# Kernel optimization log

Hardware: AMD Instinct MI355X
Metric: run time of the kernel (lower is better)

Reference implementation:

```python
import jax, jax.numpy as jnp
import numpy as np

EPS = 1e-6


def _rmsnorm(x, w, eps=EPS):
    # x: (..., d); normalize over last dim
    ms = jnp.mean(jnp.square(x), axis=-1, keepdims=True)
    return x * jax.lax.rsqrt(ms + eps) * w


def setup_inputs() -> dict:
    key = jax.random.key(0)
    ks = jax.random.split(key, 5)
    B, S, D = 2, 2048, 2048
    n_heads, n_kv = 16, 4
    d_head = D // n_heads  # 128
    sd = 1.0 / np.sqrt(D)
    return {
        "x": jax.random.normal(ks[0], (B, S, D), dtype=jnp.float32),
        "wq": jax.random.normal(ks[1], (D, n_heads * d_head), dtype=jnp.float32) * sd,
        "wk": jax.random.normal(ks[2], (D, n_kv * d_head), dtype=jnp.float32) * sd,
        "wv": jax.random.normal(ks[3], (D, n_kv * d_head), dtype=jnp.float32) * sd,
        "wo": jax.random.normal(ks[4], (D, D), dtype=jnp.float32) * sd,
        "q_norm_w": jnp.ones((d_head,), dtype=jnp.float32),
        "k_norm_w": jnp.ones((d_head,), dtype=jnp.float32),
    }


def reference(x, wq, wk, wv, wo, q_norm_w, k_norm_w):
    B, S, D = x.shape
    n_heads, n_kv = 16, 4
    groups = n_heads // n_kv
    d_head = D // n_heads

    # QKV projections (bias=False)
    q = (x @ wq).reshape(B, S, n_kv, groups, d_head)  # q heads grouped by kv head
    k = (x @ wk).reshape(B, S, n_kv, d_head)
    v = (x @ wv).reshape(B, S, n_kv, d_head)

    # qk RMSNorm over d_head
    q = _rmsnorm(q, q_norm_w)
    k = _rmsnorm(k, k_norm_w)

    # GQA attention without materializing expanded K/V:
    # scores: (B, n_kv, groups, S_q, S_k)
    scale = 1.0 / jnp.sqrt(jnp.asarray(d_head, dtype=x.dtype))
    scores = jnp.einsum('bskgd,btkd->bkgst', q, k) * scale
    causal = jnp.tril(jnp.ones((S, S), dtype=bool))
    scores = jnp.where(causal, scores, jnp.asarray(-jnp.inf, dtype=scores.dtype))
    attn = jax.nn.softmax(scores, axis=-1)
    out = jnp.einsum('bkgst,btkd->bskgd', attn, v)  # (B, S, n_kv, groups, d_head)
    out = out.reshape(B, S, D)
    return out @ wo
```

## Files before the change

kernel.cpp:

```cpp
#include <hip/hip_runtime.h>
#include <hip/hip_bf16.h>
#include <stdint.h>

typedef unsigned short u16;
typedef __attribute__((ext_vector_type(8))) short short8;
typedef __attribute__((ext_vector_type(4))) float f32x4;
typedef __attribute__((ext_vector_type(16))) float f32x16;

__device__ __forceinline__ u16 f2bf(float f){
  union { __hip_bfloat16 h; u16 u; } v; v.h = __float2bfloat16(f); return v.u;
}
__device__ __forceinline__ float bf2f(u16 h){
  union { uint32_t u; float f; } v; v.u = ((uint32_t)h) << 16;
  return v.f;
}
__device__ __forceinline__ f32x4 mfma16(short8 a, short8 b, f32x4 c){
  return __builtin_amdgcn_mfma_f32_16x16x32_bf16(a, b, c, 0, 0, 0);
}
__device__ __forceinline__ f32x16 mfma32(short8 a, short8 b, f32x16 c){
  return __builtin_amdgcn_mfma_f32_32x32x16_bf16(a, b, c, 0, 0, 0);
}
__device__ __forceinline__ void gl_lds16(const u16* g, u16* l){
  __builtin_amdgcn_global_load_lds((const __attribute__((address_space(1))) void*)g,
                                   (__attribute__((address_space(3))) void*)l, 16, 0, 0);
}
template<int N> __device__ __forceinline__ void waitvm(){
  if constexpr (N==0) asm volatile("s_waitcnt vmcnt(0)" ::: "memory");
  else if constexpr (N==2) asm volatile("s_waitcnt vmcnt(2)" ::: "memory");
  else if constexpr (N==4) asm volatile("s_waitcnt vmcnt(4)" ::: "memory");
  else if constexpr (N==8) asm volatile("s_waitcnt vmcnt(8)" ::: "memory");
  else static_assert(N==0 || N==2 || N==4 || N==8, "unsupported vmcnt");
}
__device__ __forceinline__ void phase_sep(){
  __builtin_amdgcn_sched_barrier(0);
  __builtin_amdgcn_s_barrier();
  __builtin_amdgcn_sched_barrier(0);
}
__device__ __forceinline__ uint32_t cvtpk(float lo, float hi){
  uint32_t r;
  asm("v_cvt_pk_bf16_f32 %0, %1, %2" : "=v"(r) : "v"(lo), "v"(hi));
  return r;
}

__global__ __launch_bounds__(256) void prep(const float* __restrict__ x,
    const float* __restrict__ wq, const float* __restrict__ wk,
    const float* __restrict__ wv, const float* __restrict__ wo,
    u16* __restrict__ xbf, u16* __restrict__ wqkvT, u16* __restrict__ woT)
{
  __shared__ float tile[32][33];
  int bid = blockIdx.x;
  const int tid = threadIdx.x;
  if (bid < 8192){
    const int i = bid*256 + tid;
    const float4 v = ((const float4*)x)[i];
    ushort4 pk;
    pk.x = f2bf(v.x); pk.y = f2bf(v.y); pk.z = f2bf(v.z); pk.w = f2bf(v.w);
    ((ushort4*)xbf)[i] = pk;
    return;
  }
  bid -= 8192;
  const float* src; u16* dst; int C, bx, by;
  if (bid < 4096){ src = wq; dst = wqkvT; C = 2048; bx = bid & 63; by = bid >> 6; }
  else if (bid < 8192){ bid -= 4096; src = wo; dst = woT; C = 2048; bx = bid & 63; by = bid >> 6; }
  else if (bid < 9216){ bid -= 8192; src = wk; dst = wqkvT + 2048*2048; C = 512; bx = bid & 15; by = bid >> 4; }
  else { bid -= 9216; src = wv; dst = wqkvT + 2560*2048; C = 512; bx = bid & 15; by = bid >> 4; }
  const int R = 2048;
  const int tx = tid & 31, ty = tid >> 5;
  const int c0 = bx << 5, r0 = by << 5;
  #pragma unroll
  for (int i=0;i<4;i++)
    tile[ty + (i<<3)][tx] = src[(size_t)(r0 + ty + (i<<3))*C + c0 + tx];
  __syncthreads();
  #pragma unroll
  for (int i=0;i<4;i++)
    dst[(size_t)(c0 + ty + (i<<3))*R + r0 + tx] = f2bf(tile[tx][ty + (i<<3)]);
}

__global__ __launch_bounds__(256) void v_transpose(const u16* __restrict__ qkv,
    u16* __restrict__ vT)
{
  __shared__ u16 tile[32][33];
  const int tx = threadIdx.x, ty = threadIdx.y;
  const int s0 = blockIdx.x << 5, d0 = blockIdx.y << 5;
  const int bk = blockIdx.z; const int b = bk >> 2, kv = bk & 3;
  const u16* src = qkv + (size_t)b*2048*3072 + 2560 + kv*128;
  #pragma unroll
  for (int i=0;i<4;i++)
    tile[ty + (i<<3)][tx] = src[(size_t)(s0 + ty + (i<<3))*3072 + d0 + tx];
  __syncthreads();
  u16* dst = vT + (size_t)((b<<2)+kv)*128*2048;
  #pragma unroll
  for (int i=0;i<4;i++)
    dst[(size_t)(d0 + ty + (i<<3))*2048 + s0 + tx] = tile[tx][ty + (i<<3)];
}

__global__ __launch_bounds__(256) void rmsnorm_k(u16* __restrict__ qkv,
    const float* __restrict__ kw)
{
  const int lane = threadIdx.x & 63;
  const int rid = blockIdx.x*4 + (threadIdx.x >> 6);
  const int row = rid >> 2;
  const int slot = rid & 3;
  u16* p = qkv + (size_t)row*3072 + 2048 + slot*128 + (lane<<1);
  const u16 r0 = p[0], r1 = p[1];
  const float a = bf2f(r0), c = bf2f(r1);
  float ss = a*a + c*c;
  #pragma unroll
  for (int off=1; off<64; off<<=1) ss += __shfl_xor(ss, off);
  const float sc = rsqrtf(ss*(1.0f/128.0f) + 1e-6f);
  const float w0 = kw[lane<<1], w1 = kw[(lane<<1)+1];
  p[0] = f2bf(a*sc*w0);
  p[1] = f2bf(c*sc*w1);
}

template<int BM, int CBF16>
__global__ __launch_bounds__(512, 2) void gemm8(const u16* __restrict__ A,
    const u16* __restrict__ BT, void* __restrict__ Cp,
    int M, int N, int K, int ldc)
{
  constexpr int MF   = BM/32;
  constexpr int MQ   = MF/2;
  constexpr int AH   = BM/2;
  constexpr int ASZ  = AH*64;
  constexpr int DBUF = 2*ASZ + 16384;
  constexpr int WV   = (BM==256) ? 4 : 2;
  __shared__ u16 lds[2*DBUF];
  const int tid = threadIdx.x;
  const int w = tid >> 6, lane = tid & 63;
  const int l15 = lane & 15, lg = lane >> 4;
  const int wm = w >> 2, wn = w & 3;
  const int nbx = N >> 8;
  const int nwg = gridDim.x;
  int bid = blockIdx.x;
  bid = (bid & 7) * (nwg >> 3) + (bid >> 3);
  const int m0 = (bid / nbx) * BM;
  const int n0 = (bid % nbx) << 8;

  const u16* gA0 = A  + (size_t)m0*K;
  const u16* gA1 = gA0 + (size_t)AH*K;
  const u16* gB0 = BT + (size_t)n0*K;
  const u16* gB1 = gB0 + (size_t)128*K;

  auto slotA = [&](int d, int h)->u16*{ return lds + d*DBUF + h*ASZ; };
  auto slotB = [&](int d, int h)->u16*{ return lds + d*DBUF + 2*ASZ + h*8192; };

  auto stage_half = [&](const u16* gbase, int kt, u16* sbase, int rows){
    const int iters = rows >> 6;
    for (int i=0;i<iters;i++){
      const int p = (i<<9) + tid;
      const int row = p>>3, sg = (p&7) ^ (row&7);
      gl_lds16(gbase + (size_t)row*K + (kt<<6) + (sg<<3), sbase + (p<<3));
    }
  };
  auto stA = [&](int kt, int d){ stage_half(gA0, kt, slotA(d,0), AH);
                                 stage_half(gA1, kt, slotA(d,1), AH); };
  auto stB = [&](int kt, int d){ stage_half(gB0, kt, slotB(d,0), 128);
                                 stage_half(gB1, kt, slotB(d,1), 128); };
  auto frag_at = [&](const u16* buf, int lrow, int kk)->short8{
    const int s = ((kk<<2)+lg) ^ (lrow&7);
    return *(const short8*)(buf + (((lrow<<3)+s)<<3));
  };

  short8 af[MQ][2], bfe[2][2], bfo[2][2];
  f32x4 acc[MF][4];
  #pragma unroll
  for (int m=0;m<MF;m++)
    #pragma unroll
    for (int n=0;n<4;n++) acc[m][n] = (f32x4){0.f,0.f,0.f,0.f};

  const int bh = wn>>1;
  const int brow0 = ((wn&1)<<6) + l15;

  auto rd_a = [&](const u16* buf, int mq){
    #pragma unroll
    for (int m=0;m<MQ;m++)
      #pragma unroll
      for (int kk=0;kk<2;kk++)
        af[m][kk] = frag_at(buf, mq*(BM>>2) + (m<<4) + l15, kk);
  };
  auto rd_b = [&](const u16* buf, int nq, short8 (*dst)[2]){
    #pragma unroll
    for (int n=0;n<2;n++)
      #pragma unroll
      for (int kk=0;kk<2;kk++)
        dst[n][kk] = frag_at(buf, brow0 + (nq<<5) + (n<<4), kk);
  };
  auto do_mfma = [&](int mb, int nb, short8 (*bf)[2]){
    __builtin_amdgcn_s_setprio(1);
    #pragma unroll
    for (int m=0;m<MQ;m++)
      #pragma unroll
      for (int n=0;n<2;n++)
        #pragma unroll
        for (int kk=0;kk<2;kk++)
          acc[mb+m][nb+n] = mfma16(af[m][kk], bf[n][kk], acc[mb+m][nb+n]);
    __builtin_amdgcn_s_setprio(0);
  };

  stA(0,0); stB(0,0); stA(1,1);
  waitvm<WV>();
  phase_sep();

  const int niter = K >> 7;
  for (int i=0; i<niter; ++i){
    const bool full = (i+1 < niter);
    const int t1 = 2*i+1;
    rd_a(slotA(0,wm), 0); rd_b(slotB(0,bh), 0, bfe);
    stB(t1, 1);
    phase_sep();
    do_mfma(0, 0, bfe);
    phase_sep();
    rd_b(slotB(0,bh), 1, bfo);
    phase_sep();
    do_mfma(0, 2, bfo);
    phase_sep();
    rd_a(slotA(0,wm), 1);
    phase_sep();
    do_mfma(MQ, 2, bfo);
    phase_sep();
    rd_b(slotB(0,bh), 0, bfe);
    if (full) stA(t1+1, 0);
    phase_sep();
    do_mfma(MQ, 0, bfe);
    if (full) waitvm<WV>(); else waitvm<0>();
    phase_sep();
    rd_a(slotA(1,wm), 0); rd_b(slotB(1,bh), 0, bfe);
    if (full) stB(t1+1, 0);
    phase_sep();
    do_mfma(0, 0, bfe);
    phase_sep();
    rd_b(slotB(1,bh), 1, bfo);
    phase_sep();
    do_mfma(0, 2, bfo);
    phase_sep();
    rd_a(slotA(1,wm), 1);
    phase_sep();
    do_mfma(MQ, 2, bfo);
    phase_sep();
    rd_b(slotB(1,bh), 0, bfe);
    if (full) stA(t1+2, 1);
    phase_sep();
    do_mfma(MQ, 0, bfe);
    if (full) waitvm<WV>();
    phase_sep();
  }

  #pragma unroll
  for (int m=0;m<MF;m++){
    #pragma unroll
    for (int n=0;n<4;n++){
      const int col = n0 + (wn<<6) + (n<<4) + l15;
      #pragma unroll
      for (int r=0;r<4;r++){
        const int row = m0 + wm*AH + (m<<4) + (lg<<2) + r;
        if (CBF16) ((u16*)Cp)[(size_t)row*ldc + col] = f2bf(acc[m][n][r]);
        else       ((float*)Cp)[(size_t)row*ldc + col] = acc[m][n][r];
      }
    }
  }
}

__global__ __launch_bounds__(256, 2) void attn_kernel(const u16* __restrict__ qkv,
    const u16* __restrict__ vT, const float* __restrict__ qw,
    u16* __restrict__ aout)
{
  __shared__ u16 Klds[2][8192];
  __shared__ u16 Vlds[8192];
  const int tid = threadIdx.x;
  const int w = tid >> 6, lane = tid & 63;
  const int l31 = lane & 31, hi = lane >> 5;
  const int bx = blockIdx.x, h = blockIdx.y, b = blockIdx.z;
  const int qI = b ? bx : (15 - bx);
  const int kvh = h >> 2;
  const int qb = qI*128 + (w<<5);
  const int nt = 2*qI + 2;

  const u16* qkvb = qkv + (size_t)b*2048*3072;
  short8 qf[8];
  {
    const u16* qp = qkvb + (size_t)(qb + l31)*3072 + h*128 + hi*8;
    #pragma unroll
    for (int kk=0;kk<8;kk++) qf[kk] = *(const short8*)(qp + kk*16);
    float ss = 0.f;
    #pragma unroll
    for (int kk=0;kk<8;kk++)
      #pragma unroll
      for (int e=0;e<8;e++){
        const float v = bf2f((u16)qf[kk][e]);
        ss += v*v;
      }
    ss += __shfl_xor(ss, 32);
    const float sc = rsqrtf(ss*(1.0f/128.0f) + 1e-6f) * 0.1275187952317199f;
    #pragma unroll
    for (int kk=0;kk<8;kk++){
      #pragma unroll
      for (int e=0;e<8;e++){
        const float wv_ = qw[kk*16 + hi*8 + e];
        qf[kk][e] = (short)f2bf(bf2f((u16)qf[kk][e]) * sc * wv_);
      }
    }
  }
  f32x16 oacc[4];
  #pragma unroll
  for (int d=0;d<4;d++)
    #pragma unroll
    for (int r=0;r<16;r++) oacc[d][r] = 0.f;
  float m_run = -__builtin_inff(), lsum = 0.f;

  const u16* kb_ = qkvb + 2048 + kvh*128;
  const u16* vb_ = vT + (size_t)((b<<2)+kvh)*128*2048;

  auto stageK = [&](int t, int buf){
    #pragma unroll
    for (int i=0;i<4;i++){
      const int u = (i<<8) + tid;
      const int row = u>>4, d0 = (u&15) ^ (row&15);
      gl_lds16(kb_ + (size_t)((t<<6)+row)*3072 + (d0<<3), &Klds[buf][u<<3]);
    }
  };
  auto stageV = [&](int t){
    #pragma unroll
    for (int i=0;i<4;i++){
      const int u = (i<<8) + tid;
      const int rp = u>>4, z = (u&15) ^ (rp&15);
      const int d = (rp<<1) + (z>>3), k8 = z&7;
      gl_lds16(vb_ + (size_t)d*2048 + (t<<6) + (k8<<3), &Vlds[u<<3]);
    }
  };

  stageK(0, 0);
  int kbuf = 0;
  for (int t=0; t<nt; ++t){
    const bool pre = (t+1 < nt);
    stageV(t);
    if (pre) stageK(t+1, kbuf^1);
    if (pre) waitvm<8>(); else waitvm<4>();
    phase_sep();
    const int t0 = t<<6;
    f32x16 s0, s1;
    #pragma unroll
    for (int r=0;r<16;r++){ s0[r] = 0.f; s1[r] = 0.f; }
    #pragma unroll
    for (int kk=0;kk<8;kk++){
      const int d0 = (kk<<1) + hi;
      const short8 k0 = *(const short8*)&Klds[kbuf][((l31<<4) + (d0 ^ (l31&15)))<<3];
      s0 = mfma32(k0, qf[kk], s0);
      const int r1 = 32 + l31;
      const short8 k1 = *(const short8*)&Klds[kbuf][((r1<<4) + (d0 ^ (r1&15)))<<3];
      s1 = mfma32(k1, qf[kk], s1);
    }
    if (t0 + 63 > qb){
      const int qrel = qb + l31 - t0;
      #pragma unroll
      for (int r=0;r<16;r++){
        const int kloc = (r&3) + ((r>>2)<<3) + (hi<<2);
        if (kloc      > qrel) s0[r] = -__builtin_inff();
        if (kloc + 32 > qrel) s1[r] = -__builtin_inff();
      }
    }
    float t8[8];
    #pragma unroll
    for (int i=0;i<8;i++) t8[i] = fmaxf(fmaxf(s0[i], s0[i+8]), fmaxf(s1[i], s1[i+8]));
    #pragma unroll
    for (int i=0;i<4;i++) t8[i] = fmaxf(t8[i], t8[i+4]);
    float mx = fmaxf(fmaxf(t8[0],t8[1]), fmaxf(t8[2],t8[3]));
    mx = fmaxf(mx, __shfl_xor(mx, 32));
    const bool noskip = !__all(mx - m_run <= 8.0f);
    const float mnew = noskip ? fmaxf(m_run, mx) : m_run;
    float rs = 0.f;
    #pragma unroll
    for (int i=0;i<16;i++){
      s0[i] = __builtin_amdgcn_exp2f(s0[i] - mnew);
      s1[i] = __builtin_amdgcn_exp2f(s1[i] - mnew);
      rs += s0[i] + s1[i];
    }
    rs += __shfl_xor(rs, 32);
    if (noskip){
      const float corr = __builtin_amdgcn_exp2f(m_run - mnew);
      m_run = mnew;
      lsum = lsum*corr + rs;
      #pragma unroll
      for (int r=0;r<16;r++){
        const float cr = __shfl(corr, (r&3) + ((r>>2)<<3) + (hi<<2));
        #pragma unroll
        for (int db=0;db<4;db++) oacc[db][r] *= cr;
      }
    } else {
      lsum += rs;
    }
    uint32_t paw[4][4];
    #pragma unroll
    for (int kk=0;kk<4;kk++){
      const int base = (kk&1)<<3;
      float v0,v1,v2,v3,v4,v5,v6,v7;
      if (kk<2){ v0=s0[base+0]; v1=s0[base+1]; v2=s0[base+2]; v3=s0[base+3];
                 v4=s0[base+4]; v5=s0[base+5]; v6=s0[base+6]; v7=s0[base+7]; }
      else     { v0=s1[base+0]; v1=s1[base+1]; v2=s1[base+2]; v3=s1[base+3];
                 v4=s1[base+4]; v5=s1[base+5]; v6=s1[base+6]; v7=s1[base+7]; }
      uint32_t a0 = cvtpk(v0, v1), a1 = cvtpk(v2, v3);
      uint32_t b0 = cvtpk(v4, v5), b1 = cvtpk(v6, v7);
      asm volatile("v_permlane32_swap_b32 %0, %1" : "+v"(a0), "+v"(b0));
      asm volatile("v_permlane32_swap_b32 %0, %1" : "+v"(a1), "+v"(b1));
      paw[kk][0] = a0; paw[kk][1] = a1; paw[kk][2] = b0; paw[kk][3] = b1;
    }
    if (pre) waitvm<4>(); else waitvm<0>();
    phase_sep();
    #pragma unroll
    for (int kk=0;kk<4;kk++){
      union { uint32_t w[4]; short8 v; } pu;
      pu.w[0]=paw[kk][0]; pu.w[1]=paw[kk][1]; pu.w[2]=paw[kk][2]; pu.w[3]=paw[kk][3];
      const short8 pa = pu.v;
      #pragma unroll
      for (int db=0;db<4;db++){
        const int d = (db<<5) + l31, rp = d>>1;
        const int sl = (((d&1)<<3) | ((kk<<1)+hi)) ^ (rp&15);
        const short8 vv = *(const short8*)&Vlds[((rp<<4)+sl)<<3];
        oacc[db] = mfma32(pa, vv, oacc[db]);
      }
    }
    phase_sep();
    kbuf ^= 1;
  }

  const float inv = 1.0f / lsum;
  #pragma unroll
  for (int r=0;r<16;r++){
    const int qr = (r&3) + ((r>>2)<<3) + (hi<<2);
    const float ivr = __shfl(inv, qr);
    u16* op = aout + (size_t)(b*2048 + qb + qr)*2048 + h*128 + l31;
    #pragma unroll
    for (int db=0;db<4;db++)
      op[db<<5] = f2bf(oacc[db][r] * ivr);
  }
}

extern "C" void kernel_launch(void* const* d_in, const int* in_sizes, int n_in,
                              void* d_out, int out_size, void* d_ws, size_t ws_size,
                              hipStream_t stream) {
  const float* x  = (const float*)d_in[0];
  const float* wq = (const float*)d_in[1];
  const float* wk = (const float*)d_in[2];
  const float* wv = (const float*)d_in[3];
  const float* wo = (const float*)d_in[4];
  const float* qw = (const float*)d_in[5];
  const float* kw = (const float*)d_in[6];
  char* ws = (char*)d_ws;
  u16* xbf   = (u16*)(ws);
  u16* wqkvT = (u16*)(ws + 16777216);
  u16* woT   = (u16*)(ws + 29360128);
  u16* qkv   = (u16*)(ws + 37748736);
  u16* vT    = (u16*)(ws + 62914560);
  float* out = (float*)d_out;

  prep<<<18432, 256, 0, stream>>>(x, wq, wk, wv, wo, xbf, wqkvT, woT);
  gemm8<256,1><<<192, 512, 0, stream>>>(xbf, wqkvT, qkv, 4096, 3072, 2048, 3072);
  rmsnorm_k<<<4096, 256, 0, stream>>>(qkv, kw);
  v_transpose<<<dim3(64,4,8), dim3(32,8), 0, stream>>>(qkv, vT);
  attn_kernel<<<dim3(16,16,2), 256, 0, stream>>>(qkv, vT, qw, xbf);
  gemm8<128,0><<<256, 512, 0, stream>>>(xbf, woT, out, 4096, 2048, 2048, 2048);
}
```

Before: 180.3 us.

## Use 256x192-tile QKV GEMM kernel so 256 workgroups fill all CUs

Adds a dedicated GEMM kernel for the QKV projection with a 256x192 output tile. This gives 256 workgroups instead of 192 for the 4096x3072 problem, matching the CU count better and reducing tail imbalance. The kernel interleaves even and odd B-fragment MFMA phases with a hand-scheduled double-buffered LDS pipeline. Each wave now does a 48-wide N slice, giving a different register and LDS footprint that could affect occupancy.

Result: faster. 175.0 us (-3.0%).

```diff
diff --git a/kernel.cpp b/kernel.cpp
--- a/kernel.cpp
+++ b/kernel.cpp
@@ -111,6 +111,166 @@
   const float w0 = kw[lane<<1], w1 = kw[(lane<<1)+1];
   p[0] = f2bf(a*sc*w0);
   p[1] = f2bf(c*sc*w1);
+}
+
+__global__ __launch_bounds__(512, 2) void gemm192(const u16* __restrict__ A,
+    const u16* __restrict__ BT, u16* __restrict__ Cp,
+    int M, int N, int K, int ldc)
+{
+  constexpr int ASZ  = 128*64;
+  constexpr int BSZ  = 64*64;
+  constexpr int DBUF = 2*ASZ + 3*BSZ;
+  __shared__ u16 lds[2*DBUF];
+  const int tid = threadIdx.x;
+  const int w = tid >> 6, lane = tid & 63;
+  const int l15 = lane & 15, lg = lane >> 4;
+  const int wm = w >> 2, wn = w & 3;
+  const int nbx = N / 192;
+  const int nwg = gridDim.x;
+  int bid = blockIdx.x;
+  bid = (bid & 7) * (nwg >> 3) + (bid >> 3);
+  const int m0 = (bid / nbx) << 8;
+  const int n0 = (bid % nbx) * 192;
+
+  const u16* gA0 = A  + (size_t)m0*K;
+  const u16* gA1 = gA0 + (size_t)128*K;
+  const u16* gB  = BT + (size_t)n0*K;
+
+  auto slotA = [&](int d, int h)->u16*{ return lds + d*DBUF + h*ASZ; };
+  auto slotB = [&](int d, int s)->u16*{ return lds + d*DBUF + 2*ASZ + s*BSZ; };
+
+  auto stage128 = [&](const u16* gbase, int kt, u16* sbase){
+    #pragma unroll
+    for (int i=0;i<2;i++){
+      const int p = (i<<9) + tid;
+      const int row = p>>3, sg = (p&7) ^ (row&7);
+      gl_lds16(gbase + (size_t)row*K + (kt<<6) + (sg<<3), sbase + (p<<3));
+    }
+  };
+  auto stage64 = [&](const u16* gbase, int kt, u16* sbase){
+    const int row = tid>>3, sg = (tid&7) ^ (row&7);
+    gl_lds16(gbase + (size_t)row*K + (kt<<6) + (sg<<3), sbase + (tid<<3));
+  };
+  auto stA = [&](int kt, int d){ stage128(gA0, kt, slotA(d,0));
+                                 stage128(gA1, kt, slotA(d,1)); };
+  auto stB = [&](int kt, int d){ stage64(gB,               kt, slotB(d,0));
+                                 stage64(gB + (size_t) 64*K, kt, slotB(d,1));
+                                 stage64(gB + (size_t)128*K, kt, slotB(d,2)); };
+  auto frag_at = [&](const u16* buf, int lrow, int kk)->short8{
+    const int s = ((kk<<2)+lg) ^ (lrow&7);
+    return *(const short8*)(buf + (((lrow<<3)+s)<<3));
+  };
+
+  short8 af[4][2], bfe[2][2], bfo[2];
+  f32x4 acc[8][3];
+  #pragma unroll
+  for (int m=0;m<8;m++)
+    #pragma unroll
+    for (int n=0;n<3;n++) acc[m][n] = (f32x4){0.f,0.f,0.f,0.f};
+
+  auto rd_a = [&](int d, int mq){
+    #pragma unroll
+    for (int m=0;m<4;m++)
+      #pragma unroll
+      for (int kk=0;kk<2;kk++)
+        af[m][kk] = frag_at(slotA(d,wm), (mq<<6) + (m<<4) + l15, kk);
+  };
+  auto rd_be = [&](int d){
+    #pragma unroll
+    for (int n=0;n<2;n++){
+      const int r = wn*48 + (n<<4) + l15;
+      #pragma unroll
+      for (int kk=0;kk<2;kk++)
+        bfe[n][kk] = frag_at(slotB(d, r>>6), r&63, kk);
+    }
+  };
+  auto rd_bo = [&](int d){
+    const int r = wn*48 + 32 + l15;
+    #pragma unroll
+    for (int kk=0;kk<2;kk++)
+      bfo[kk] = frag_at(slotB(d, r>>6), r&63, kk);
+  };
+  auto mf_e = [&](int mb){
+    __builtin_amdgcn_s_setprio(1);
+    #pragma unroll
+    for (int m=0;m<4;m++)
+      #pragma unroll
+      for (int n=0;n<2;n++)
+        #pragma unroll
+        for (int kk=0;kk<2;kk++)
+          acc[mb+m][n] = mfma16(af[m][kk], bfe[n][kk], acc[mb+m][n]);
+    __builtin_amdgcn_s_setprio(0);
+  };
+  auto mf_o = [&](int mb){
+    __builtin_amdgcn_s_setprio(1);
+    #pragma unroll
+    for (int m=0;m<4;m++)
+      #pragma unroll
+      for (int kk=0;kk<2;kk++)
+        acc[mb+m][2] = mfma16(af[m][kk], bfo[kk], acc[mb+m][2]);
+    __builtin_amdgcn_s_setprio(0);
+  };
+
+  stA(0,0); stB(0,0); stA(1,1);
+  waitvm<4>();
+  phase_sep();
+
+  const int niter = K >> 7;
+  for (int i=0; i<niter; ++i){
+    const bool full = (i+1 < niter);
+    const int t1 = 2*i+1;
+    rd_a(0, 0); rd_be(0);
+    stB(t1, 1);
+    phase_sep();
+    mf_e(0);
+    phase_sep();
+    rd_bo(0);
+    phase_sep();
+    mf_o(0);
+    phase_sep();
+    rd_a(0, 1);
+    phase_sep();
+    mf_o(4);
+    phase_sep();
+    rd_be(0);
+    if (full) stA(t1+1, 0);
+    phase_sep();
+    mf_e(4);
+    if (full) waitvm<4>(); else waitvm<0>();
+    phase_sep();
+    rd_a(1, 0); rd_be(1);
+    if (full) stB(t1+1, 0);
+    phase_sep();
+    mf_e(0);
+    phase_sep();
+    rd_bo(1);
+    phase_sep();
+    mf_o(0);
+    phase_sep();
+    rd_a(1, 1);
+    phase_sep();
+    mf_o(4);
+    phase_sep();
+    rd_be(1);
+    if (full) stA(t1+2, 1);
+    phase_sep();
+    mf_e(4);
+    if (full) waitvm<4>();
+    phase_sep();
+  }
+
+  #pragma unroll
+  for (int m=0;m<8;m++){
+    #pragma unroll
+    for (int n=0;n<3;n++){
+      const int col = n0 + wn*48 + (n<<4) + l15;
+      #pragma unroll
+      for (int r=0;r<4;r++){
+        const int row = m0 + (wm<<7) + (m<<4) + (lg<<2) + r;
+        Cp[(size_t)row*ldc + col] = f2bf(acc[m][n][r]);
+      }
+    }
+  }
 }
 
 template<int BM, int CBF16>
@@ -453,7 +613,7 @@
   float* out = (float*)d_out;
 
   prep<<<18432, 256, 0, stream>>>(x, wq, wk, wv, wo, xbf, wqkvT, woT);
-  gemm8<256,1><<<192, 512, 0, stream>>>(xbf, wqkvT, qkv, 4096, 3072, 2048, 3072);
+  gemm192<<<256, 512, 0, stream>>>(xbf, wqkvT, qkv, 4096, 3072, 2048, 3072);
   rmsnorm_k<<<4096, 256, 0, stream>>>(qkv, kw);
   v_transpose<<<dim3(64,4,8), dim3(32,8), 0, stream>>>(qkv, vT);
   attn_kernel<<<dim3(16,16,2), 256, 0, stream>>>(qkv, vT, qw, xbf);
```
